# Optimization experiments

Hardware: AMD Instinct MI355X
Metric: run time of the kernel (lower is better)

Reference implementation:

```python
import jax, jax.numpy as jnp
import numpy as np

THRESH = 0.999  # dynamic outlier percentile

# Standard NF4 signpost values (normalized to [-1, 1])
NF4 = np.array([-1.0, -0.6961928009986877, -0.5250730514526367, -0.39491748809814453,
                -0.28444138169288635, -0.18477343022823334, -0.09105003625154495, 0.0,
                0.07958029955625534, 0.16093020141124725, 0.24611230194568634, 0.33791524171829224,
                0.44070982933044434, 0.5626170039176941, 0.7229568362236023, 1.0], dtype=np.float32)


def setup_inputs() -> dict:
    key = jax.random.key(0)
    k1, k2 = jax.random.split(key)
    x = jax.random.normal(k1, (4096, 4096), dtype=jnp.float32)        # [tokens, in_features]
    weight = jax.random.normal(k2, (4096, 4096), dtype=jnp.float32)   # [out_features, in_features]
    nf_lut = jnp.asarray(NF4)                                          # [16] NF4 poles
    return {"x": x, "weight": weight, "nf_lut": nf_lut}


def quantize_nf(weight, nf_lut):
    # --- dynamic outlier detection (get_outliers_dynamic, qchannel=-1) ---
    t = 1.0 - (1.0 - THRESH) / 2.0
    upper = jnp.quantile(weight, t, axis=-1, keepdims=True)        # [R,1]
    lower = jnp.quantile(weight, 1.0 - t, axis=-1, keepdims=True)  # [R,1]
    outlier_mask = (weight <= lower) | (weight >= upper)           # [R,C] bool

    # --- include_sparse scale computation (quant_fn_nf) ---
    outliers0 = weight * outlier_mask
    median = jnp.median(weight, axis=-1, keepdims=True)
    tmp = weight - outliers0 + median * outlier_mask               # outliers replaced by median
    maxval = jnp.max(tmp, axis=-1, keepdims=True)
    minval = jnp.min(tmp, axis=-1, keepdims=True)
    offset = (maxval + minval) * 0.5
    rangeval = (maxval - minval) * 0.5

    w = weight - offset
    outliers = w * outlier_mask        # sparse (fp) component
    w = w - outliers                   # dense component
    w_scaled = w / rangeval            # normalized to ~[-1, 1]

    # --- nearest-pole (NF) rounding: argmin over |w - pole| ---
    idx = jnp.argmin(jnp.abs(w_scaled[..., None] - nf_lut), axis=-1)  # [R,C]
    Q = nf_lut[idx].astype(jnp.float16).astype(jnp.float32)           # .half() in torch

    # --- dequant ---
    qw = Q * rangeval + outliers + offset
    qw = jnp.nan_to_num(qw, nan=0.0, posinf=0.0, neginf=0.0)
    return qw


def reference(x, weight, nf_lut):
    qweight = quantize_nf(weight, nf_lut)   # simulated NF4 dense+sparse dequant
    return x @ qweight.T                    # [tokens, out_features]
```

## Files before the change

kernel.cpp:

```cpp
#include <hip/hip_runtime.h>
#include <hip/hip_fp16.h>
#include <stdint.h>

typedef __attribute__((ext_vector_type(4))) float f32x4;
typedef __attribute__((ext_vector_type(8))) short short8;

__device__ __forceinline__ unsigned short f2bf(float f) {
  unsigned int b = __float_as_uint(f);
  b = b + 0x7FFFu + ((b >> 16) & 1u);
  return (unsigned short)(b >> 16);
}

#define CE(a, b) { float _lo = fminf((a), (b)), _hi = fmaxf((a), (b)); (a) = _lo; (b) = _hi; }

__device__ __forceinline__ void merge8(float x[8]) {
  CE(x[0], x[4]); CE(x[1], x[5]); CE(x[2], x[6]); CE(x[3], x[7]);
  CE(x[2], x[4]); CE(x[3], x[5]);
  CE(x[1], x[2]); CE(x[3], x[4]); CE(x[5], x[6]);
}

__global__ __launch_bounds__(256) void prep_kernel(const float* __restrict__ x,
                                                   const float* __restrict__ W,
                                                   const float* __restrict__ lut,
                                                   unsigned short* __restrict__ xb,
                                                   unsigned short* __restrict__ qb) {
  const int tid = threadIdx.x;

  if (blockIdx.x >= 4096) {
    int b = blockIdx.x - 4096;
    int base = b * 1024 + tid;
#pragma unroll
    for (int it = 0; it < 4; ++it) {
      int i = base + it * 256;
      f32x4 v = ((const f32x4*)x)[i];
      ushort4 u;
      u.x = f2bf(v[0]); u.y = f2bf(v[1]); u.z = f2bf(v[2]); u.w = f2bf(v[3]);
      ((ushort4*)xb)[i] = u;
    }
    return;
  }

  const int C = 4096;
  const int row = blockIdx.x;
  const int lane = tid & 63;
  const int wv = tid >> 6;

  __shared__ float s_luth[16];
  __shared__ float s_mid[15];
  __shared__ float s_red[4][8];
  __shared__ float s_par[4];

  if (tid < 16) {
    float f = lut[tid];
    s_luth[tid] = __half2float(__float2half(f));
  }
  if (tid < 15) s_mid[tid] = 0.5f * (lut[tid] + lut[tid + 1]);

  const f32x4* Wp = (const f32x4*)(W + (size_t)row * C);
  f32x4 v[4];
#pragma unroll
  for (int i = 0; i < 4; ++i) v[i] = Wp[i * 256 + tid];

  float bot[4] = {__builtin_inff(), __builtin_inff(), __builtin_inff(), __builtin_inff()};
  float top[4] = {-__builtin_inff(), -__builtin_inff(), -__builtin_inff(), -__builtin_inff()};
#pragma unroll
  for (int i = 0; i < 4; ++i) {
#pragma unroll
    for (int j = 0; j < 4; ++j) {
      float f = v[i][j];
      bot[3] = fminf(bot[3], f); CE(bot[2], bot[3]); CE(bot[1], bot[2]); CE(bot[0], bot[1]);
      top[0] = fmaxf(top[0], f); CE(top[0], top[1]); CE(top[1], top[2]); CE(top[2], top[3]);
    }
  }

#pragma unroll
  for (int d = 1; d < 64; d <<= 1) {
    float xx[8];
#pragma unroll
    for (int j = 0; j < 4; ++j) { xx[j] = bot[j]; xx[4 + j] = __shfl_xor(bot[j], d); }
    merge8(xx);
#pragma unroll
    for (int j = 0; j < 4; ++j) bot[j] = xx[j];
#pragma unroll
    for (int j = 0; j < 4; ++j) { xx[j] = top[j]; xx[4 + j] = __shfl_xor(top[j], d); }
    merge8(xx);
#pragma unroll
    for (int j = 0; j < 4; ++j) top[j] = xx[4 + j];
  }

  if (lane == 0) {
#pragma unroll
    for (int j = 0; j < 4; ++j) { s_red[wv][j] = bot[j]; s_red[wv][4 + j] = top[j]; }
  }
  __syncthreads();

  if (tid == 0) {
    float a[8], b[8], m[8];
#pragma unroll
    for (int j = 0; j < 4; ++j) { a[j] = s_red[0][j]; a[4 + j] = s_red[1][j]; }
    merge8(a);
#pragma unroll
    for (int j = 0; j < 4; ++j) { b[j] = s_red[2][j]; b[4 + j] = s_red[3][j]; }
    merge8(b);
#pragma unroll
    for (int j = 0; j < 4; ++j) { m[j] = a[j]; m[4 + j] = b[j]; }
    merge8(m);
    float lower = m[2] + 0.0475f * (m[3] - m[2]);
#pragma unroll
    for (int j = 0; j < 4; ++j) { a[j] = s_red[0][4 + j]; a[4 + j] = s_red[1][4 + j]; }
    merge8(a);
#pragma unroll
    for (int j = 0; j < 4; ++j) { b[j] = s_red[2][4 + j]; b[4 + j] = s_red[3][4 + j]; }
    merge8(b);
#pragma unroll
    for (int j = 0; j < 4; ++j) { m[j] = a[4 + j]; m[4 + j] = b[4 + j]; }
    merge8(m);
    float upper = m[4] + 0.9525f * (m[5] - m[4]);
    s_par[0] = lower; s_par[1] = upper;
  }
  __syncthreads();

  float lower = s_par[0], upper = s_par[1];

  float mn = __builtin_inff(), mx = -__builtin_inff();
#pragma unroll
  for (int i = 0; i < 4; ++i) {
#pragma unroll
    for (int j = 0; j < 4; ++j) {
      float f = v[i][j];
      bool outl = (f <= lower) || (f >= upper);
      if (!outl) { mn = fminf(mn, f); mx = fmaxf(mx, f); }
    }
  }
#pragma unroll
  for (int d = 1; d < 64; d <<= 1) {
    mn = fminf(mn, __shfl_xor(mn, d));
    mx = fmaxf(mx, __shfl_xor(mx, d));
  }
  if (lane == 0) { s_red[wv][0] = mn; s_red[wv][1] = mx; }
  __syncthreads();
  if (tid == 0) {
    float tmn = fminf(fminf(s_red[0][0], s_red[1][0]), fminf(s_red[2][0], s_red[3][0]));
    float tmx = fmaxf(fmaxf(s_red[0][1], s_red[1][1]), fmaxf(s_red[2][1], s_red[3][1]));
    s_par[2] = (tmx + tmn) * 0.5f;
    s_par[3] = (tmx - tmn) * 0.5f;
  }
  __syncthreads();
  float offset = s_par[2], range = s_par[3];
  float invr = 1.0f / range;

  unsigned short* outr = qb + (size_t)row * C;
#pragma unroll
  for (int i = 0; i < 4; ++i) {
    ushort4 o;
    unsigned short os[4];
#pragma unroll
    for (int j = 0; j < 4; ++j) {
      float f = v[i][j];
      bool outl = (f <= lower) || (f >= upper);
      float q;
      if (outl) {
        q = f;
      } else {
        float ws = (f - offset) * invr;
        int bi = (ws > s_mid[7]) ? 8 : 0;
        bi += (ws > s_mid[bi + 3]) ? 4 : 0;
        bi += (ws > s_mid[bi + 1]) ? 2 : 0;
        bi += (ws > s_mid[bi]) ? 1 : 0;
        q = s_luth[bi] * range + offset;
      }
      if (!isfinite(q)) q = 0.0f;
      os[j] = f2bf(q);
    }
    o.x = os[0]; o.y = os[1]; o.z = os[2]; o.w = os[3];
    ((ushort4*)outr)[i * 256 + tid] = o;
  }
}

#define GK 4096

__device__ __forceinline__ void gload16(const void* gp, void* lp) {
  __builtin_amdgcn_global_load_lds(
      (const __attribute__((address_space(1))) unsigned int*)(uintptr_t)gp,
      (__attribute__((address_space(3))) unsigned int*)(unsigned int)(uintptr_t)lp,
      16, 0, 0);
}

#define BAR()    __builtin_amdgcn_s_barrier()
#define SCHED0() __builtin_amdgcn_sched_barrier(0)
#define LGKM0()  asm volatile("s_waitcnt lgkmcnt(0)" ::: "memory")
#define VM6()    asm volatile("s_waitcnt vmcnt(6)" ::: "memory")
#define PRIO1()  __builtin_amdgcn_s_setprio(1)
#define PRIO0()  __builtin_amdgcn_s_setprio(0)

__global__ __launch_bounds__(512, 2) void gemm_bt(const unsigned short* __restrict__ A,
                                                  const unsigned short* __restrict__ B,
                                                  float* __restrict__ C) {
  __shared__ __align__(16) unsigned short sA[2][2][8192];
  __shared__ __align__(16) unsigned short sB[2][2][8192];

  const int tid = threadIdx.x;
  const int lane = tid & 63;
  const int wv = tid >> 6;
  const int wm = wv >> 2, wn = wv & 3;
  const int fr = lane & 15, fk = lane >> 4;

  int bi = blockIdx.x;
  int swz = (bi & 7) * 32 + (bi >> 3);
  int brow = swz >> 4, bcol = swz & 15;

  const unsigned short* Abase = A + (size_t)brow * 256 * GK;
  const unsigned short* Bbase = B + (size_t)bcol * 256 * GK;

  const int cA = (fk * 16) ^ ((fr & 8) << 2);

  const int srow = (wv >> 1) * 16 + (lane >> 2);
  const int skelt = ((wv & 1) * 64 + (((lane & 3) * 16) ^ ((lane & 32) ? 32 : 0))) >> 1;

  auto stage = [&](const unsigned short* gb, unsigned short* lb, int h, int kt) {
    const unsigned short* g = gb + ((size_t)h * 128) * GK + kt * 64 + skelt;
    char* lc = (char*)lb + wv * 1024 + lane * 16;
#pragma unroll
    for (int l = 0; l < 2; ++l)
      gload16(g + (size_t)(l * 64 + srow) * GK, lc + l * 8192);
  };

  f32x4 acc[8][4];
#pragma unroll
  for (int m = 0; m < 8; ++m)
#pragma unroll
    for (int n = 0; n < 4; ++n) acc[m][n] = (f32x4){0.f, 0.f, 0.f, 0.f};

  stage(Abase, &sA[0][0][0], 0, 0);
  stage(Abase, &sA[0][1][0], 1, 0);
  stage(Bbase, &sB[0][0][0], 0, 0);
  stage(Bbase, &sB[0][1][0], 1, 0);
  stage(Bbase, &sB[1][0][0], 0, 1);
  stage(Bbase, &sB[1][1][0], 1, 1);
  stage(Abase, &sA[1][0][0], 0, 1);
  VM6();
  BAR();
  SCHED0();

  const int nsub = (wn & 1) * 4;

#pragma unroll 1
  for (int i = 0; i < 32; ++i) {
    const int ktA1 = 2 * i + 1;
    const int ktN0 = (2 * i + 2 < 64) ? 2 * i + 2 : 63;
    const int ktN1 = (2 * i + 3 < 64) ? 2 * i + 3 : 63;

    short8 af[4][2], bf0[2][2], bf1[2][2];

    {
      const char* bA = (const char*)&sA[0][wm][0];
      const char* bB = (const char*)&sB[0][wn >> 1][0];

#pragma unroll
      for (int m = 0; m < 4; ++m)
#pragma unroll
        for (int kh = 0; kh < 2; ++kh)
          af[m][kh] = *(const short8*)(bA + m * 2048 + kh * 1024 + fr * 64 + cA);
#pragma unroll
      for (int n = 0; n < 2; ++n)
#pragma unroll
        for (int kh = 0; kh < 2; ++kh)
          bf0[n][kh] = *(const short8*)(bB + (nsub + n) * 2048 + kh * 1024 + fr * 64 + cA);
      stage(Abase, &sA[1][1][0], 1, ktA1);
      BAR(); LGKM0(); SCHED0(); PRIO1();
#pragma unroll
      for (int m = 0; m < 4; ++m)
#pragma unroll
        for (int n = 0; n < 2; ++n)
#pragma unroll
          for (int kh = 0; kh < 2; ++kh)
            acc[m][n] = __builtin_amdgcn_mfma_f32_16x16x32_bf16(af[m][kh], bf0[n][kh], acc[m][n], 0, 0, 0);
      PRIO0(); SCHED0(); BAR();

#pragma unroll
      for (int n = 0; n < 2; ++n)
#pragma unroll
        for (int kh = 0; kh < 2; ++kh)
          bf1[n][kh] = *(const short8*)(bB + (nsub + n + 2) * 2048 + kh * 1024 + fr * 64 + cA);
      BAR(); LGKM0(); SCHED0(); PRIO1();
#pragma unroll
      for (int m = 0; m < 4; ++m)
#pragma unroll
        for (int n = 0; n < 2; ++n)
#pragma unroll
          for (int kh = 0; kh < 2; ++kh)
            acc[m][n + 2] = __builtin_amdgcn_mfma_f32_16x16x32_bf16(af[m][kh], bf1[n][kh], acc[m][n + 2], 0, 0, 0);
      PRIO0(); SCHED0(); BAR();

#pragma unroll
      for (int m = 0; m < 4; ++m)
#pragma unroll
        for (int kh = 0; kh < 2; ++kh)
          af[m][kh] = *(const short8*)(bA + (m + 4) * 2048 + kh * 1024 + fr * 64 + cA);
      stage(Bbase, &sB[0][0][0], 0, ktN0);
      BAR(); LGKM0(); SCHED0(); PRIO1();
#pragma unroll
      for (int m = 0; m < 4; ++m)
#pragma unroll
        for (int n = 0; n < 2; ++n)
#pragma unroll
          for (int kh = 0; kh < 2; ++kh)
            acc[m + 4][n + 2] = __builtin_amdgcn_mfma_f32_16x16x32_bf16(af[m][kh], bf1[n][kh], acc[m + 4][n + 2], 0, 0, 0);
      PRIO0(); SCHED0(); BAR();

      stage(Bbase, &sB[0][1][0], 1, ktN0);
      stage(Abase, &sA[0][0][0], 0, ktN0);
      BAR(); PRIO1();
#pragma unroll
      for (int m = 0; m < 4; ++m)
#pragma unroll
        for (int n = 0; n < 2; ++n)
#pragma unroll
          for (int kh = 0; kh < 2; ++kh)
            acc[m + 4][n] = __builtin_amdgcn_mfma_f32_16x16x32_bf16(af[m][kh], bf0[n][kh], acc[m + 4][n], 0, 0, 0);
      PRIO0(); SCHED0();
      VM6(); BAR(); SCHED0();
    }

    {
      const char* bA = (const char*)&sA[1][wm][0];
      const char* bB = (const char*)&sB[1][wn >> 1][0];

#pragma unroll
      for (int m = 0; m < 4; ++m)
#pragma unroll
        for (int kh = 0; kh < 2; ++kh)
          af[m][kh] = *(const short8*)(bA + m * 2048 + kh * 1024 + fr * 64 + cA);
#pragma unroll
      for (int n = 0; n < 2; ++n)
#pragma unroll
        for (int kh = 0; kh < 2; ++kh)
          bf0[n][kh] = *(const short8*)(bB + (nsub + n) * 2048 + kh * 1024 + fr * 64 + cA);
      stage(Abase, &sA[0][1][0], 1, ktN0);
      BAR(); LGKM0(); SCHED0(); PRIO1();
#pragma unroll
      for (int m = 0; m < 4; ++m)
#pragma unroll
        for (int n = 0; n < 2; ++n)
#pragma unroll
          for (int kh = 0; kh < 2; ++kh)
            acc[m][n] = __builtin_amdgcn_mfma_f32_16x16x32_bf16(af[m][kh], bf0[n][kh], acc[m][n], 0, 0, 0);
      PRIO0(); SCHED0(); BAR();

#pragma unroll
      for (int n = 0; n < 2; ++n)
#pragma unroll
        for (int kh = 0; kh < 2; ++kh)
          bf1[n][kh] = *(const short8*)(bB + (nsub + n + 2) * 2048 + kh * 1024 + fr * 64 + cA);
      BAR(); LGKM0(); SCHED0(); PRIO1();
#pragma unroll
      for (int m = 0; m < 4; ++m)
#pragma unroll
        for (int n = 0; n < 2; ++n)
#pragma unroll
          for (int kh = 0; kh < 2; ++kh)
            acc[m][n + 2] = __builtin_amdgcn_mfma_f32_16x16x32_bf16(af[m][kh], bf1[n][kh], acc[m][n + 2], 0, 0, 0);
      PRIO0(); SCHED0(); BAR();

#pragma unroll
      for (int m = 0; m < 4; ++m)
#pragma unroll
        for (int kh = 0; kh < 2; ++kh)
          af[m][kh] = *(const short8*)(bA + (m + 4) * 2048 + kh * 1024 + fr * 64 + cA);
      stage(Bbase, &sB[1][0][0], 0, ktN1);
      BAR(); LGKM0(); SCHED0(); PRIO1();
#pragma unroll
      for (int m = 0; m < 4; ++m)
#pragma unroll
        for (int n = 0; n < 2; ++n)
#pragma unroll
          for (int kh = 0; kh < 2; ++kh)
            acc[m + 4][n + 2] = __builtin_amdgcn_mfma_f32_16x16x32_bf16(af[m][kh], bf1[n][kh], acc[m + 4][n + 2], 0, 0, 0);
      PRIO0(); SCHED0(); BAR();

      stage(Bbase, &sB[1][1][0], 1, ktN1);
      stage(Abase, &sA[1][0][0], 0, ktN1);
      BAR(); PRIO1();
#pragma unroll
      for (int m = 0; m < 4; ++m)
#pragma unroll
        for (int n = 0; n < 2; ++n)
#pragma unroll
          for (int kh = 0; kh < 2; ++kh)
            acc[m + 4][n] = __builtin_amdgcn_mfma_f32_16x16x32_bf16(af[m][kh], bf0[n][kh], acc[m + 4][n], 0, 0, 0);
      PRIO0(); SCHED0();
      VM6(); BAR(); SCHED0();
    }
  }

  const int rbase = brow * 256 + wm * 128;
  const int cbase = bcol * 256 + wn * 64;
#pragma unroll
  for (int m = 0; m < 8; ++m)
#pragma unroll
    for (int n = 0; n < 4; ++n)
#pragma unroll
      for (int j = 0; j < 4; ++j) {
        int rr = rbase + m * 16 + fk * 4 + j;
        int cc = cbase + n * 16 + fr;
        C[(size_t)rr * GK + cc] = acc[m][n][j];
      }
}

extern "C" void kernel_launch(void* const* d_in, const int* in_sizes, int n_in,
                              void* d_out, int out_size, void* d_ws, size_t ws_size,
                              hipStream_t stream) {
  const float* x = (const float*)d_in[0];
  const float* W = (const float*)d_in[1];
  const float* lut = (const float*)d_in[2];
  float* out = (float*)d_out;

  unsigned short* xb = (unsigned short*)d_ws;
  unsigned short* qb = xb + (size_t)4096 * 4096;

  prep_kernel<<<8192, 256, 0, stream>>>(x, W, lut, xb, qb);
  gemm_bt<<<256, 512, 0, stream>>>(xb, qb, out);
}
```

Before: 155.5 us.

## Switch GEMM to 32x32x16 MFMA with new LDS layout and staging order

Replaces the 16x16x32 bf16 MFMA tiles with 32x32x16 MFMA, restructuring the accumulators into 4x2 f32x16 blocks. Fragment reads, the LDS swizzle and the global-to-LDS staging row mapping are rewritten to match the 32-row fragment layout. The A-tile prefetch is moved into the first sub-phase of each half-iteration, and the vmcnt wait is adjusted to match. Larger MFMA tiles reduce LDS reads per flop and instruction count, at the risk of bank conflicts or a less effective overlap schedule.

```diff
diff --git a/kernel.cpp b/kernel.cpp
--- a/kernel.cpp
+++ b/kernel.cpp
@@ -3,6 +3,7 @@
 #include <stdint.h>
 
 typedef __attribute__((ext_vector_type(4))) float f32x4;
+typedef __attribute__((ext_vector_type(16))) float f32x16;
 typedef __attribute__((ext_vector_type(8))) short short8;
 
 __device__ __forceinline__ unsigned short f2bf(float f) {
@@ -189,7 +190,7 @@
 #define BAR()    __builtin_amdgcn_s_barrier()
 #define SCHED0() __builtin_amdgcn_sched_barrier(0)
 #define LGKM0()  asm volatile("s_waitcnt lgkmcnt(0)" ::: "memory")
-#define VM6()    asm volatile("s_waitcnt vmcnt(6)" ::: "memory")
+#define VM4()    asm volatile("s_waitcnt vmcnt(4)" ::: "memory")
 #define PRIO1()  __builtin_amdgcn_s_setprio(1)
 #define PRIO0()  __builtin_amdgcn_s_setprio(0)
 
@@ -203,7 +204,7 @@
   const int lane = tid & 63;
   const int wv = tid >> 6;
   const int wm = wv >> 2, wn = wv & 3;
-  const int fr = lane & 15, fk = lane >> 4;
+  const int nrg = (wn & 1) * 2;
 
   int bi = blockIdx.x;
   int swz = (bi & 7) * 32 + (bi >> 3);
@@ -212,24 +213,28 @@
   const unsigned short* Abase = A + (size_t)brow * 256 * GK;
   const unsigned short* Bbase = B + (size_t)bcol * 256 * GK;
 
-  const int cA = (fk * 16) ^ ((fr & 8) << 2);
-
-  const int srow = (wv >> 1) * 16 + (lane >> 2);
-  const int skelt = ((wv & 1) * 64 + (((lane & 3) * 16) ^ ((lane & 32) ? 32 : 0))) >> 1;
+  const int r64 = (lane & 31) * 64;
+  const int s0 = ((lane >> 5) << 4) ^ ((lane & 24) << 1);
+
+  const int srow = ((wv & 1) << 4) + (lane >> 2);
+  const int skelt = (((((wv >> 1) & 1) << 6)
+                    | ((((lane & 3) << 4) ^ ((lane & 32) ? 16 : 0) ^ ((wv & 1) ? 32 : 0)))) >> 1);
 
   auto stage = [&](const unsigned short* gb, unsigned short* lb, int h, int kt) {
     const unsigned short* g = gb + ((size_t)h * 128) * GK + kt * 64 + skelt;
     char* lc = (char*)lb + wv * 1024 + lane * 16;
 #pragma unroll
     for (int l = 0; l < 2; ++l)
-      gload16(g + (size_t)(l * 64 + srow) * GK, lc + l * 8192);
+      gload16(g + (size_t)((l * 2 + (wv >> 2)) * 32 + srow) * GK, lc + l * 8192);
   };
 
-  f32x4 acc[8][4];
-#pragma unroll
-  for (int m = 0; m < 8; ++m)
-#pragma unroll
-    for (int n = 0; n < 4; ++n) acc[m][n] = (f32x4){0.f, 0.f, 0.f, 0.f};
+  f32x16 acc[4][2];
+#pragma unroll
+  for (int mb = 0; mb < 4; ++mb)
+#pragma unroll
+    for (int nb = 0; nb < 2; ++nb)
+#pragma unroll
+      for (int r = 0; r < 16; ++r) acc[mb][nb][r] = 0.0f;
 
   stage(Abase, &sA[0][0][0], 0, 0);
   stage(Abase, &sA[0][1][0], 1, 0);
@@ -237,12 +242,9 @@
   stage(Bbase, &sB[0][1][0], 1, 0);
   stage(Bbase, &sB[1][0][0], 0, 1);
   stage(Bbase, &sB[1][1][0], 1, 1);
-  stage(Abase, &sA[1][0][0], 0, 1);
-  VM6();
+  VM4();
   BAR();
   SCHED0();
-
-  const int nsub = (wn & 1) * 4;
 
 #pragma unroll 1
   for (int i = 0; i < 32; ++i) {
@@ -250,76 +252,64 @@
     const int ktN0 = (2 * i + 2 < 64) ? 2 * i + 2 : 63;
     const int ktN1 = (2 * i + 3 < 64) ? 2 * i + 3 : 63;
 
-    short8 af[4][2], bf0[2][2], bf1[2][2];
+    short8 afL[2][4], afH[2][4], bf0[4], bf1[4];
 
     {
       const char* bA = (const char*)&sA[0][wm][0];
       const char* bB = (const char*)&sB[0][wn >> 1][0];
 
 #pragma unroll
-      for (int m = 0; m < 4; ++m)
-#pragma unroll
-        for (int kh = 0; kh < 2; ++kh)
-          af[m][kh] = *(const short8*)(bA + m * 2048 + kh * 1024 + fr * 64 + cA);
-#pragma unroll
-      for (int n = 0; n < 2; ++n)
-#pragma unroll
-        for (int kh = 0; kh < 2; ++kh)
-          bf0[n][kh] = *(const short8*)(bB + (nsub + n) * 2048 + kh * 1024 + fr * 64 + cA);
+      for (int mb = 0; mb < 2; ++mb)
+#pragma unroll
+        for (int ks = 0; ks < 4; ++ks)
+          afL[mb][ks] = *(const short8*)(bA + mb * 4096 + (ks >> 1) * 2048 + r64 + (s0 ^ ((ks & 1) << 5)));
+#pragma unroll
+      for (int ks = 0; ks < 4; ++ks)
+        bf0[ks] = *(const short8*)(bB + nrg * 4096 + (ks >> 1) * 2048 + r64 + (s0 ^ ((ks & 1) << 5)));
+      stage(Abase, &sA[1][0][0], 0, ktA1);
+      BAR(); LGKM0(); SCHED0(); PRIO1();
+#pragma unroll
+      for (int mb = 0; mb < 2; ++mb)
+#pragma unroll
+        for (int ks = 0; ks < 4; ++ks)
+          acc[mb][0] = __builtin_amdgcn_mfma_f32_32x32x16_bf16(afL[mb][ks], bf0[ks], acc[mb][0], 0, 0, 0);
+      PRIO0(); SCHED0(); BAR();
+
+#pragma unroll
+      for (int ks = 0; ks < 4; ++ks)
+        bf1[ks] = *(const short8*)(bB + (nrg + 1) * 4096 + (ks >> 1) * 2048 + r64 + (s0 ^ ((ks & 1) << 5)));
       stage(Abase, &sA[1][1][0], 1, ktA1);
       BAR(); LGKM0(); SCHED0(); PRIO1();
 #pragma unroll
-      for (int m = 0; m < 4; ++m)
-#pragma unroll
-        for (int n = 0; n < 2; ++n)
-#pragma unroll
-          for (int kh = 0; kh < 2; ++kh)
-            acc[m][n] = __builtin_amdgcn_mfma_f32_16x16x32_bf16(af[m][kh], bf0[n][kh], acc[m][n], 0, 0, 0);
-      PRIO0(); SCHED0(); BAR();
-
-#pragma unroll
-      for (int n = 0; n < 2; ++n)
-#pragma unroll
-        for (int kh = 0; kh < 2; ++kh)
-          bf1[n][kh] = *(const short8*)(bB + (nsub + n + 2) * 2048 + kh * 1024 + fr * 64 + cA);
-      BAR(); LGKM0(); SCHED0(); PRIO1();
-#pragma unroll
-      for (int m = 0; m < 4; ++m)
-#pragma unroll
-        for (int n = 0; n < 2; ++n)
-#pragma unroll
-          for (int kh = 0; kh < 2; ++kh)
-            acc[m][n + 2] = __builtin_amdgcn_mfma_f32_16x16x32_bf16(af[m][kh], bf1[n][kh], acc[m][n + 2], 0, 0, 0);
-      PRIO0(); SCHED0(); BAR();
-
-#pragma unroll
-      for (int m = 0; m < 4; ++m)
-#pragma unroll
-        for (int kh = 0; kh < 2; ++kh)
-          af[m][kh] = *(const short8*)(bA + (m + 4) * 2048 + kh * 1024 + fr * 64 + cA);
+      for (int mb = 0; mb < 2; ++mb)
+#pragma unroll
+        for (int ks = 0; ks < 4; ++ks)
+          acc[mb][1] = __builtin_amdgcn_mfma_f32_32x32x16_bf16(afL[mb][ks], bf1[ks], acc[mb][1], 0, 0, 0);
+      PRIO0(); SCHED0(); BAR();
+
+#pragma unroll
+      for (int mb = 0; mb < 2; ++mb)
+#pragma unroll
+        for (int ks = 0; ks < 4; ++ks)
+          afH[mb][ks] = *(const short8*)(bA + (mb + 2) * 4096 + (ks >> 1) * 2048 + r64 + (s0 ^ ((ks & 1) << 5)));
       stage(Bbase, &sB[0][0][0], 0, ktN0);
       BAR(); LGKM0(); SCHED0(); PRIO1();
 #pragma unroll
-      for (int m = 0; m < 4; ++m)
-#pragma unroll
-        for (int n = 0; n < 2; ++n)
-#pragma unroll
-          for (int kh = 0; kh < 2; ++kh)
-            acc[m + 4][n + 2] = __builtin_amdgcn_mfma_f32_16x16x32_bf16(af[m][kh], bf1[n][kh], acc[m + 4][n + 2], 0, 0, 0);
+      for (int mb = 0; mb < 2; ++mb)
+#pragma unroll
+        for (int ks = 0; ks < 4; ++ks)
+          acc[mb + 2][1] = __builtin_amdgcn_mfma_f32_32x32x16_bf16(afH[mb][ks], bf1[ks], acc[mb + 2][1], 0, 0, 0);
       PRIO0(); SCHED0(); BAR();
 
       stage(Bbase, &sB[0][1][0], 1, ktN0);
-      stage(Abase, &sA[0][0][0], 0, ktN0);
       BAR(); PRIO1();
 #pragma unroll
-      for (int m = 0; m < 4; ++m)
-#pragma unroll
-        for (int n = 0; n < 2; ++n)
-#pragma unroll
-          for (int kh = 0; kh < 2; ++kh)
-            acc[m + 4][n] = __builtin_amdgcn_mfma_f32_16x16x32_bf16(af[m][kh], bf0[n][kh], acc[m + 4][n], 0, 0, 0);
+      for (int mb = 0; mb < 2; ++mb)
+#pragma unroll
+        for (int ks = 0; ks < 4; ++ks)
+          acc[mb + 2][0] = __builtin_amdgcn_mfma_f32_32x32x16_bf16(afH[mb][ks], bf0[ks], acc[mb + 2][0], 0, 0, 0);
       PRIO0(); SCHED0();
-      VM6(); BAR(); SCHED0();
+      VM4(); BAR(); SCHED0();
     }
 
     {
@@ -327,83 +317,72 @@
       const char* bB = (const char*)&sB[1][wn >> 1][0];
 
 #pragma unroll
-      for (int m = 0; m < 4; ++m)
-#pragma unroll
-        for (int kh = 0; kh < 2; ++kh)
-          af[m][kh] = *(const short8*)(bA + m * 2048 + kh * 1024 + fr * 64 + cA);
-#pragma unroll
-      for (int n = 0; n < 2; ++n)
-#pragma unroll
-        for (int kh = 0; kh < 2; ++kh)
-          bf0[n][kh] = *(const short8*)(bB + (nsub + n) * 2048 + kh * 1024 + fr * 64 + cA);
+      for (int mb = 0; mb < 2; ++mb)
+#pragma unroll
+        for (int ks = 0; ks < 4; ++ks)
+          afL[mb][ks] = *(const short8*)(bA + mb * 4096 + (ks >> 1) * 2048 + r64 + (s0 ^ ((ks & 1) << 5)));
+#pragma unroll
+      for (int ks = 0; ks < 4; ++ks)
+        bf0[ks] = *(const short8*)(bB + nrg * 4096 + (ks >> 1) * 2048 + r64 + (s0 ^ ((ks & 1) << 5)));
+      stage(Abase, &sA[0][0][0], 0, ktN0);
+      BAR(); LGKM0(); SCHED0(); PRIO1();
+#pragma unroll
+      for (int mb = 0; mb < 2; ++mb)
+#pragma unroll
+        for (int ks = 0; ks < 4; ++ks)
+          acc[mb][0] = __builtin_amdgcn_mfma_f32_32x32x16_bf16(afL[mb][ks], bf0[ks], acc[mb][0], 0, 0, 0);
+      PRIO0(); SCHED0(); BAR();
+
+#pragma unroll
+      for (int ks = 0; ks < 4; ++ks)
+        bf1[ks] = *(const short8*)(bB + (nrg + 1) * 4096 + (ks >> 1) * 2048 + r64 + (s0 ^ ((ks & 1) << 5)));
       stage(Abase, &sA[0][1][0], 1, ktN0);
       BAR(); LGKM0(); SCHED0(); PRIO1();
 #pragma unroll
-      for (int m = 0; m < 4; ++m)
-#pragma unroll
-        for (int n = 0; n < 2; ++n)
-#pragma unroll
-          for (int kh = 0; kh < 2; ++kh)
-            acc[m][n] = __builtin_amdgcn_mfma_f32_16x16x32_bf16(af[m][kh], bf0[n][kh], acc[m][n], 0, 0, 0);
-      PRIO0(); SCHED0(); BAR();
-
-#pragma unroll
-      for (int n = 0; n < 2; ++n)
-#pragma unroll
-        for (int kh = 0; kh < 2; ++kh)
-          bf1[n][kh] = *(const short8*)(bB + (nsub + n + 2) * 2048 + kh * 1024 + fr * 64 + cA);
-      BAR(); LGKM0(); SCHED0(); PRIO1();
-#pragma unroll
-      for (int m = 0; m < 4; ++m)
-#pragma unroll
-        for (int n = 0; n < 2; ++n)
-#pragma unroll
-          for (int kh = 0; kh < 2; ++kh)
-            acc[m][n + 2] = __builtin_amdgcn_mfma_f32_16x16x32_bf16(af[m][kh], bf1[n][kh], acc[m][n + 2], 0, 0, 0);
-      PRIO0(); SCHED0(); BAR();
-
-#pragma unroll
-      for (int m = 0; m < 4; ++m)
-#pragma unroll
-        for (int kh = 0; kh < 2; ++kh)
-          af[m][kh] = *(const short8*)(bA + (m + 4) * 2048 + kh * 1024 + fr * 64 + cA);
+      for (int mb = 0; mb < 2; ++mb)
+#pragma unroll
+        for (int ks = 0; ks < 4; ++ks)
+          acc[mb][1] = __builtin_amdgcn_mfma_f32_32x32x16_bf16(afL[mb][ks], bf1[ks], acc[mb][1], 0, 0, 0);
+      PRIO0(); SCHED0(); BAR();
+
+#pragma unroll
+      for (int mb = 0; mb < 2; ++mb)
+#pragma unroll
+        for (int ks = 0; ks < 4; ++ks)
+          afH[mb][ks] = *(const short8*)(bA + (mb + 2) * 4096 + (ks >> 1) * 2048 + r64 + (s0 ^ ((ks & 1) << 5)));
       stage(Bbase, &sB[1][0][0], 0, ktN1);
       BAR(); LGKM0(); SCHED0(); PRIO1();
 #pragma unroll
-      for (int m = 0; m < 4; ++m)
-#pragma unroll
-        for (int n = 0; n < 2; ++n)
-#pragma unroll
-          for (int kh = 0; kh < 2; ++kh)
-            acc[m + 4][n + 2] = __builtin_amdgcn_mfma_f32_16x16x32_bf16(af[m][kh], bf1[n][kh], acc[m + 4][n + 2], 0, 0, 0);
+      for (int mb = 0; mb < 2; ++mb)
+#pragma unroll
+        for (int ks = 0; ks < 4; ++ks)
+          acc[mb + 2][1] = __builtin_amdgcn_mfma_f32_32x32x16_bf16(afH[mb][ks], bf1[ks], acc[mb + 2][1], 0, 0, 0);
       PRIO0(); SCHED0(); BAR();
 
       stage(Bbase, &sB[1][1][0], 1, ktN1);
-      stage(Abase, &sA[1][0][0], 0, ktN1);
       BAR(); PRIO1();
 #pragma unroll
-      for (int m = 0; m < 4; ++m)
-#pragma unroll
-        for (int n = 0; n < 2; ++n)
-#pragma unroll
-          for (int kh = 0; kh < 2; ++kh)
-            acc[m + 4][n] = __builtin_amdgcn_mfma_f32_16x16x32_bf16(af[m][kh], bf0[n][kh], acc[m + 4][n], 0, 0, 0);
+      for (int mb = 0; mb < 2; ++mb)
+#pragma unroll
+        for (int ks = 0; ks < 4; ++ks)
+          acc[mb + 2][0] = __builtin_amdgcn_mfma_f32_32x32x16_bf16(afH[mb][ks], bf0[ks], acc[mb + 2][0], 0, 0, 0);
       PRIO0(); SCHED0();
-      VM6(); BAR(); SCHED0();
-    }
-  }
-
-  const int rbase = brow * 256 + wm * 128;
-  const int cbase = bcol * 256 + wn * 64;
-#pragma unroll
-  for (int m = 0; m < 8; ++m)
-#pragma unroll
-    for (int n = 0; n < 4; ++n)
-#pragma unroll
-      for (int j = 0; j < 4; ++j) {
-        int rr = rbase + m * 16 + fk * 4 + j;
-        int cc = cbase + n * 16 + fr;
-        C[(size_t)rr * GK + cc] = acc[m][n][j];
+      VM4(); BAR(); SCHED0();
+    }
+  }
+
+  const int rb0 = brow * 256 + wm * 128;
+  const int cb0 = bcol * 256 + wn * 64 + (lane & 31);
+  const int rhi = (lane >> 5) * 4;
+#pragma unroll
+  for (int mb = 0; mb < 4; ++mb)
+#pragma unroll
+    for (int nb = 0; nb < 2; ++nb)
+#pragma unroll
+      for (int reg = 0; reg < 16; ++reg) {
+        int rr = rb0 + mb * 32 + (reg & 3) + 8 * (reg >> 2) + rhi;
+        int cc = cb0 + nb * 32;
+        C[(size_t)rr * GK + cc] = acc[mb][nb][reg];
       }
 }
 
```

Result: slower. 164.5 us (+5.8%).
